# Performance work log

Hardware: AMD Instinct MI355X
Metric: run time of the kernel (lower is better)

Reference implementation:

```python
import jax, jax.numpy as jnp
import numpy as np

KH, KW = 3, 3      # kernel_size
SH, SW = 1, 1      # stride
MINVAL, MAXVAL = -0.45, -0.15


def setup_inputs() -> dict:
    key = jax.random.key(0)
    kx, kw = jax.random.split(key)
    x = jax.random.normal(kx, (16, 128, 128, 16), dtype=jnp.float32)  # NHWC
    W = jax.random.uniform(kw, (KH, KW, 16, 32), minval=MINVAL, maxval=MAXVAL,
                           dtype=jnp.float32)  # [kh, kw, C_in, filters]
    return {"x": x, "W": W}


def _dilation(x, W):
    # Max-plus sliding-window 'convolution' (VALID padding):
    # out[b,i,j,f] = max_{di,dj,c} x[b, i*SH+di, j*SW+dj, c] + W[di,dj,c,f]
    kh, kw, C, F = W.shape
    B, H, Wd, _ = x.shape
    Hout = (H - kh) // SH + 1
    Wout = (Wd - kw) // SW + 1
    out = jnp.full((B, Hout, Wout, F), -jnp.inf, dtype=x.dtype)
    for di in range(kh):          # small fixed loop over kernel offsets
        for dj in range(kw):
            xs = x[:, di:di + Hout * SH:SH, dj:dj + Wout * SW:SW, :]  # [B,Hout,Wout,C]
            # add W for this offset, reduce max over input channels
            out = jnp.maximum(out, jnp.max(xs[..., :, None] + W[di, dj], axis=3))
    return out


def reference(x, W):
    # erosion(x) = -dilation(-x)
    return -_dilation(-x, W)
```

## Files before the change

### kernel.cpp

```cpp
#include <hip/hip_runtime.h>
#include <math.h>


#define TI 21
#define TROWS (TI + 2)
#define LROW 64

typedef _Float16 h2 __attribute__((ext_vector_type(2)));

__device__ __forceinline__ h2 hmin2(h2 a, h2 b) {
    return __builtin_elementwise_min(a, b);
}

__device__ __forceinline__ h2 pkrtz(float a, float b) {
    auto r = __builtin_amdgcn_cvt_pkrtz(a, b);
    return *reinterpret_cast<h2*>(&r);
}

__device__ __forceinline__ h2 rowmin3(const float4* pr, const h2 w[3][4]) {
    h2 t[12];
#pragma unroll
    for (int dj = 0; dj < 3; ++dj) {
        const h2* p = reinterpret_cast<const h2*>(&pr[dj]);
#pragma unroll
        for (int q = 0; q < 4; ++q)
            t[dj * 4 + q] = p[q] - w[dj][q];
    }
#pragma unroll
    for (int k = 0; k < 6; ++k) t[k] = hmin2(t[k], t[k + 6]);
    t[0] = hmin2(t[0], t[3]);
    t[1] = hmin2(t[1], t[4]);
    t[2] = hmin2(t[2], t[5]);
    return hmin2(hmin2(t[0], t[1]), t[2]);
}

__global__ __launch_bounds__(256) void erosion_kernel(
    const float* __restrict__ x, const float* __restrict__ Wt,
    float* __restrict__ out)
{
    __shared__ _Float16 tile[2 * TROWS * LROW];
    __shared__ _Float16 wvm[TI * 256];

    const int tid = threadIdx.x;
    const int f  = tid & 31;
    const int ch = (tid >> 5) & 1;
    const int jt = tid >> 6;
    const int b  = blockIdx.z;
    const int i0 = blockIdx.y * TI;
    const int jb = blockIdx.x * 4;

    {
        const float* xg = x + (size_t)b * (128 * 128 * 16);
        auto stage = [&](int t) {
            int r   = t / 12;
            int k   = t % 12;
            int cc  = k >> 1;
            int ch2 = k & 1;
            int col = min(jb + cc, 127);
            const float* src = xg + ((size_t)(i0 + r) * 128 + col) * 16 + ch2 * 8;
            float4 lo = *reinterpret_cast<const float4*>(src);
            float4 hi = *reinterpret_cast<const float4*>(src + 4);
            h2 o[4] = { pkrtz(lo.x, lo.y), pkrtz(lo.z, lo.w),
                        pkrtz(hi.x, hi.y), pkrtz(hi.z, hi.w) };
            *reinterpret_cast<float4*>(
                &tile[ch2 * (TROWS * LROW) + r * LROW + cc * 8]) =
                *reinterpret_cast<float4*>(o);
        };
        stage(tid);
        if (tid < TROWS * 12 - 256) stage(tid + 256);
    }

    {
        h2* wl = reinterpret_cast<h2*>(wvm);
#pragma unroll
        for (int rr = 0; rr < 9; ++rr) {
            int t  = rr * 256 + tid;
            int g  = t >> 5;
            int ff = t & 31;
            float a  = Wt[g * 64 + ff];
            float c2 = Wt[g * 64 + 32 + ff];
            wl[g * 32 + ff] = pkrtz(a, c2);
        }
    }

    __syncthreads();

    h2 wh[3][3][4];
    {
        const h2* wl = reinterpret_cast<const h2*>(wvm);
#pragma unroll
        for (int p = 0; p < 9; ++p)
#pragma unroll
            for (int q = 0; q < 4; ++q)
                wh[p / 3][p % 3][q] = wl[(p * 8 + ch * 4 + q) * 32 + f];
    }

    const _Float16* lb = &tile[ch * (TROWS * LROW) + jt * 8];

    float4 pre[3];
#pragma unroll
    for (int dj = 0; dj < 3; ++dj)
        pre[dj] = *reinterpret_cast<const float4*>(lb + dj * 8);

    __syncthreads();

    const _Float16 HINF = (_Float16)__builtin_huge_valf();
    h2 accB = {HINF, HINF};
    h2 accC = {HINF, HINF};

    auto body = [&](int r, bool do_prefetch, bool do_vm) {
        h2 n0 = rowmin3(pre, wh[0]);
        h2 n1 = rowmin3(pre, wh[1]);
        h2 n2 = rowmin3(pre, wh[2]);

        if (do_prefetch) {
            const _Float16* ln = lb + (r + 1) * LROW;
#pragma unroll
            for (int dj = 0; dj < 3; ++dj)
                pre[dj] = *reinterpret_cast<const float4*>(ln + dj * 8);
        }

        h2 fin2 = hmin2(accC, n2);
        accC = hmin2(accB, n1);
        accB = n0;

        if (do_vm) {
            _Float16 a = fin2[0], c = fin2[1];
            _Float16 vm = a < c ? a : c;
            wvm[(r - 2) * 256 + tid] = vm;
        }
    };

    body(0, true, false);
    body(1, true, false);
#pragma unroll
    for (int r = 2; r < TROWS - 1; ++r)
        body(r, true, true);
    body(TROWS - 1, false, true);

    __syncthreads();

    {
        float* outb = out + (size_t)b * (126 * 126 * 32);
        auto merge = [&](int t) {
            int row = t >> 5;
            int k   = t & 31;
            int col = k >> 3;
            int q   = k & 7;
            int jj  = jb + col;
            const _Float16* base = &wvm[row * 256 + col * 64 + q * 4];
            h2 a[2], c[2];
            *reinterpret_cast<double*>(a) = *reinterpret_cast<const double*>(base);
            *reinterpret_cast<double*>(c) = *reinterpret_cast<const double*>(base + 32);
            h2 m0 = hmin2(a[0], c[0]);
            h2 m1 = hmin2(a[1], c[1]);
            float4 o = { (float)m0[0], (float)m0[1], (float)m1[0], (float)m1[1] };
            if (jj < 126)
                *reinterpret_cast<float4*>(
                    &outb[((size_t)(i0 + row) * 126 + jj) * 32 + q * 4]) = o;
        };
        merge(tid);
        merge(tid + 256);
        if (tid < TI * 32 - 512) merge(tid + 512);
    }
}

extern "C" void kernel_launch(void* const* d_in, const int* in_sizes, int n_in,
                              void* d_out, int out_size, void* d_ws, size_t ws_size,
                              hipStream_t stream) {
    const float* x  = (const float*)d_in[0];
    const float* Wt = (const float*)d_in[1];
    float* out = (float*)d_out;

    dim3 grid(32, 6, 16);
    dim3 block(256);
    erosion_kernel<<<grid, block, 0, stream>>>(x, Wt, out);
}
```

Before: 108.3 us.

## Widen blocks to 8 columns and store outputs directly via cross-lane min

Doubles the block to 512 threads covering 8 output columns per block, which halves the grid and lowers the overlap of staged halo columns. The LDS stage that merged the two channel halves is replaced by a permlane32 swap (or a shfl_xor fallback) that reduces the halves in registers, and results are written straight to global memory from the compute loop. This removes the extra LDS round trip and one barrier. In exchange the stores become scalar 4-byte writes issued by only half the lanes, and the larger blocks with launch-bounds occupancy hints may constrain register allocation.

Measured after the change: 184.9 us. 1.71x slower.

```diff
diff --git a/kernel.cpp b/kernel.cpp
--- a/kernel.cpp
+++ b/kernel.cpp
@@ -4,7 +4,9 @@
 
 #define TI 21
 #define TROWS (TI + 2)
-#define LROW 64
+#define NCOL 8
+#define SCOL 10
+#define LROW 80
 
 typedef _Float16 h2 __attribute__((ext_vector_type(2)));
 
@@ -34,12 +36,12 @@
     return hmin2(hmin2(t[0], t[1]), t[2]);
 }
 
-__global__ __launch_bounds__(256) void erosion_kernel(
+__global__ __launch_bounds__(512, 8) void erosion_kernel(
     const float* __restrict__ x, const float* __restrict__ Wt,
     float* __restrict__ out)
 {
-    __shared__ _Float16 tile[2 * TROWS * LROW];
-    __shared__ _Float16 wvm[TI * 256];
+    __shared__ __align__(16) _Float16 tile[2 * TROWS * LROW];
+    __shared__ __align__(16) _Float16 wbuf[2 * 2304];
 
     const int tid = threadIdx.x;
     const int f  = tid & 31;
@@ -47,39 +49,39 @@
     const int jt = tid >> 6;
     const int b  = blockIdx.z;
     const int i0 = blockIdx.y * TI;
-    const int jb = blockIdx.x * 4;
+    const int jb = blockIdx.x * NCOL;
 
-    {
+    if (tid < TROWS * 2 * SCOL) {
         const float* xg = x + (size_t)b * (128 * 128 * 16);
-        auto stage = [&](int t) {
-            int r   = t / 12;
-            int k   = t % 12;
-            int cc  = k >> 1;
-            int ch2 = k & 1;
-            int col = min(jb + cc, 127);
-            const float* src = xg + ((size_t)(i0 + r) * 128 + col) * 16 + ch2 * 8;
-            float4 lo = *reinterpret_cast<const float4*>(src);
-            float4 hi = *reinterpret_cast<const float4*>(src + 4);
-            h2 o[4] = { pkrtz(lo.x, lo.y), pkrtz(lo.z, lo.w),
-                        pkrtz(hi.x, hi.y), pkrtz(hi.z, hi.w) };
-            *reinterpret_cast<float4*>(
-                &tile[ch2 * (TROWS * LROW) + r * LROW + cc * 8]) =
-                *reinterpret_cast<float4*>(o);
-        };
-        stage(tid);
-        if (tid < TROWS * 12 - 256) stage(tid + 256);
+        int r   = tid / (2 * SCOL);
+        int k   = tid % (2 * SCOL);
+        int cc  = k >> 1;
+        int ch2 = k & 1;
+        int col = min(jb + cc, 127);
+        const float* src = xg + ((size_t)(i0 + r) * 128 + col) * 16 + ch2 * 8;
+        float4 lo = *reinterpret_cast<const float4*>(src);
+        float4 hi = *reinterpret_cast<const float4*>(src + 4);
+        h2 o[4] = { pkrtz(lo.x, lo.y), pkrtz(lo.z, lo.w),
+                    pkrtz(hi.x, hi.y), pkrtz(hi.z, hi.w) };
+        *reinterpret_cast<float4*>(
+            &tile[ch2 * (TROWS * LROW) + r * LROW + cc * 8]) =
+            *reinterpret_cast<float4*>(o);
     }
 
     {
-        h2* wl = reinterpret_cast<h2*>(wvm);
+        h2* wl = reinterpret_cast<h2*>(wbuf);
 #pragma unroll
-        for (int rr = 0; rr < 9; ++rr) {
-            int t  = rr * 256 + tid;
+        for (int rr = 0; rr < 4; ++rr) {
+            int t  = rr * 512 + tid;
             int g  = t >> 5;
             int ff = t & 31;
-            float a  = Wt[g * 64 + ff];
-            float c2 = Wt[g * 64 + 32 + ff];
-            wl[g * 32 + ff] = pkrtz(a, c2);
+            wl[t] = pkrtz(Wt[g * 64 + ff], Wt[g * 64 + 32 + ff]);
+        }
+        if (tid < 2304 - 2048) {
+            int t  = 2048 + tid;
+            int g  = t >> 5;
+            int ff = t & 31;
+            wl[t] = pkrtz(Wt[g * 64 + ff], Wt[g * 64 + 32 + ff]);
         }
     }
 
@@ -87,7 +89,7 @@
 
     h2 wh[3][3][4];
     {
-        const h2* wl = reinterpret_cast<const h2*>(wvm);
+        const h2* wl = reinterpret_cast<const h2*>(wbuf);
 #pragma unroll
         for (int p = 0; p < 9; ++p)
 #pragma unroll
@@ -102,13 +104,15 @@
     for (int dj = 0; dj < 3; ++dj)
         pre[dj] = *reinterpret_cast<const float4*>(lb + dj * 8);
 
-    __syncthreads();
-
     const _Float16 HINF = (_Float16)__builtin_huge_valf();
     h2 accB = {HINF, HINF};
     h2 accC = {HINF, HINF};
 
-    auto body = [&](int r, bool do_prefetch, bool do_vm) {
+    const int jj = jb + jt;
+    const bool wr = (ch == 0) && (jj < 126);
+    float* outb = out + (size_t)b * (126 * 126 * 32) + (size_t)jj * 32 + f;
+
+    auto body = [&](int r, bool do_prefetch, bool do_store) {
         h2 n0 = rowmin3(pre, wh[0]);
         h2 n1 = rowmin3(pre, wh[1]);
         h2 n2 = rowmin3(pre, wh[2]);
@@ -124,10 +128,19 @@
         accC = hmin2(accB, n1);
         accB = n0;
 
-        if (do_vm) {
-            _Float16 a = fin2[0], c = fin2[1];
-            _Float16 vm = a < c ? a : c;
-            wvm[(r - 2) * 256 + tid] = vm;
+        if (do_store) {
+            unsigned ua = __builtin_bit_cast(unsigned, fin2);
+#if __has_builtin(__builtin_amdgcn_permlane32_swap)
+            auto sw = __builtin_amdgcn_permlane32_swap(ua, ua, false, false);
+            h2 m2 = hmin2(__builtin_bit_cast(h2, (unsigned)sw[0]),
+                          __builtin_bit_cast(h2, (unsigned)sw[1]));
+#else
+            unsigned ub = (unsigned)__shfl_xor((int)ua, 32, 64);
+            h2 m2 = hmin2(fin2, __builtin_bit_cast(h2, ub));
+#endif
+            _Float16 m = m2[0] < m2[1] ? m2[0] : m2[1];
+            if (wr)
+                outb[(size_t)(i0 + r - 2) * (126 * 32)] = (float)m;
         }
     };
 
@@ -137,32 +150,6 @@
     for (int r = 2; r < TROWS - 1; ++r)
         body(r, true, true);
     body(TROWS - 1, false, true);
-
-    __syncthreads();
-
-    {
-        float* outb = out + (size_t)b * (126 * 126 * 32);
-        auto merge = [&](int t) {
-            int row = t >> 5;
-            int k   = t & 31;
-            int col = k >> 3;
-            int q   = k & 7;
-            int jj  = jb + col;
-            const _Float16* base = &wvm[row * 256 + col * 64 + q * 4];
-            h2 a[2], c[2];
-            *reinterpret_cast<double*>(a) = *reinterpret_cast<const double*>(base);
-            *reinterpret_cast<double*>(c) = *reinterpret_cast<const double*>(base + 32);
-            h2 m0 = hmin2(a[0], c[0]);
-            h2 m1 = hmin2(a[1], c[1]);
-            float4 o = { (float)m0[0], (float)m0[1], (float)m1[0], (float)m1[1] };
-            if (jj < 126)
-                *reinterpret_cast<float4*>(
-                    &outb[((size_t)(i0 + row) * 126 + jj) * 32 + q * 4]) = o;
-        };
-        merge(tid);
-        merge(tid + 256);
-        if (tid < TI * 32 - 512) merge(tid + 512);
-    }
 }
 
 extern "C" void kernel_launch(void* const* d_in, const int* in_sizes, int n_in,
@@ -172,7 +159,7 @@
     const float* Wt = (const float*)d_in[1];
     float* out = (float*)d_out;
 
-    dim3 grid(32, 6, 16);
-    dim3 block(256);
+    dim3 grid(16, 6, 16);
+    dim3 block(512);
     erosion_kernel<<<grid, block, 0, stream>>>(x, Wt, out);
 }
```

## Switch erosion inner loop to fp32 with v_min3, 512 threads and cross-lane merge

Applied to the files above, without the earlier changes.

Replaces the packed fp16 compute path with fp32 arithmetic that uses v_min3_f32, and doubles the block to 512 threads so each thread handles a quarter of the channels. Partial minima are merged across wave halves with permlane32_swap or a shuffle before the results go to LDS. The tile and weight buffers are now kept in fp32 with a padded layout, and the weights are read with inline ds_read_b128. The row loop is software-pipelined with two prefetch buffers. This is meant to drop the fp16 conversions and raise parallelism, at the cost of more LDS and more threads per output.

Measured after the change: 115.8 us. 6.9% more time.

```diff
diff --git a/kernel.cpp b/kernel.cpp
--- a/kernel.cpp
+++ b/kernel.cpp
@@ -4,7 +4,12 @@
 
 #define TI 21
 #define TROWS (TI + 2)
-#define LROW 64
+#define NCOL 4
+#define SCOL 6
+#define TROWF 96
+#define WPF 640
+#define VROW 288
+#define VGRP 36
 
 typedef _Float16 h2 __attribute__((ext_vector_type(2)));
 
@@ -12,131 +17,183 @@
     return __builtin_elementwise_min(a, b);
 }
 
-__device__ __forceinline__ h2 pkrtz(float a, float b) {
-    auto r = __builtin_amdgcn_cvt_pkrtz(a, b);
-    return *reinterpret_cast<h2*>(&r);
-}
-
-__device__ __forceinline__ h2 rowmin3(const float4* pr, const h2 w[3][4]) {
-    h2 t[12];
+__device__ __forceinline__ float min3f(float a, float b, float c) {
+    float d;
+    asm("v_min3_f32 %0, %1, %2, %3" : "=v"(d) : "v"(a), "v"(b), "v"(c));
+    return d;
+}
+
+__device__ __forceinline__ float rowminf(const float4* pr, const float4* w) {
+    float s[12];
 #pragma unroll
     for (int dj = 0; dj < 3; ++dj) {
-        const h2* p = reinterpret_cast<const h2*>(&pr[dj]);
-#pragma unroll
-        for (int q = 0; q < 4; ++q)
-            t[dj * 4 + q] = p[q] - w[dj][q];
-    }
-#pragma unroll
-    for (int k = 0; k < 6; ++k) t[k] = hmin2(t[k], t[k + 6]);
-    t[0] = hmin2(t[0], t[3]);
-    t[1] = hmin2(t[1], t[4]);
-    t[2] = hmin2(t[2], t[5]);
-    return hmin2(hmin2(t[0], t[1]), t[2]);
-}
-
-__global__ __launch_bounds__(256) void erosion_kernel(
+        const float* p = reinterpret_cast<const float*>(&pr[dj]);
+        const float* q = reinterpret_cast<const float*>(&w[dj]);
+#pragma unroll
+        for (int j = 0; j < 4; ++j)
+            s[dj * 4 + j] = p[j] - q[j];
+    }
+    float g0 = min3f(s[0], s[1], s[2]);
+    float g1 = min3f(s[3], s[4], s[5]);
+    float g2 = min3f(s[6], s[7], s[8]);
+    float g3 = min3f(s[9], s[10], s[11]);
+    return fminf(min3f(g0, g1, g2), g3);
+}
+
+__device__ __forceinline__ float mergev(float v) {
+    unsigned u = __builtin_bit_cast(unsigned, v);
+#if __has_builtin(__builtin_amdgcn_permlane32_swap)
+    auto sw = __builtin_amdgcn_permlane32_swap(u, u, false, false);
+    return fminf(__builtin_bit_cast(float, (unsigned)sw[0]),
+                 __builtin_bit_cast(float, (unsigned)sw[1]));
+#else
+    unsigned ub = (unsigned)__shfl_xor((int)u, 32, 64);
+    return fminf(v, __builtin_bit_cast(float, ub));
+#endif
+}
+
+__global__ __launch_bounds__(512)
+__attribute__((amdgpu_waves_per_eu(4, 4)))
+void erosion_kernel(
     const float* __restrict__ x, const float* __restrict__ Wt,
     float* __restrict__ out)
 {
-    __shared__ _Float16 tile[2 * TROWS * LROW];
-    __shared__ _Float16 wvm[TI * 256];
+    __shared__ __align__(16) float    tileF[TROWS * TROWF];
+    __shared__ __align__(16) float    wbufF[9 * WPF];
+    __shared__ __align__(16) _Float16 vm[TI * VROW];
 
     const int tid = threadIdx.x;
-    const int f  = tid & 31;
-    const int ch = (tid >> 5) & 1;
-    const int jt = tid >> 6;
+    const int f   = tid & 31;
+    const int chq = (tid >> 5) & 3;
+    const int jt  = tid >> 7;
+    const int src = (tid >> 6) & 1;
     const int b  = blockIdx.z;
     const int i0 = blockIdx.y * TI;
-    const int jb = blockIdx.x * 4;
+    const int jb = blockIdx.x * NCOL;
 
     {
         const float* xg = x + (size_t)b * (128 * 128 * 16);
         auto stage = [&](int t) {
-            int r   = t / 12;
-            int k   = t % 12;
-            int cc  = k >> 1;
-            int ch2 = k & 1;
+            int r  = t / 24;
+            int k  = t % 24;
+            int cc = k >> 2;
+            int cg = k & 3;
             int col = min(jb + cc, 127);
-            const float* src = xg + ((size_t)(i0 + r) * 128 + col) * 16 + ch2 * 8;
-            float4 lo = *reinterpret_cast<const float4*>(src);
-            float4 hi = *reinterpret_cast<const float4*>(src + 4);
-            h2 o[4] = { pkrtz(lo.x, lo.y), pkrtz(lo.z, lo.w),
-                        pkrtz(hi.x, hi.y), pkrtz(hi.z, hi.w) };
-            *reinterpret_cast<float4*>(
-                &tile[ch2 * (TROWS * LROW) + r * LROW + cc * 8]) =
-                *reinterpret_cast<float4*>(o);
+            const float* s = xg + ((size_t)(i0 + r) * 128 + col) * 16 + cg * 4;
+            *reinterpret_cast<float4*>(&tileF[r * TROWF + cc * 16 + cg * 4]) =
+                *reinterpret_cast<const float4*>(s);
         };
         stage(tid);
-        if (tid < TROWS * 12 - 256) stage(tid + 256);
-    }
-
-    {
-        h2* wl = reinterpret_cast<h2*>(wvm);
+        if (tid < TROWS * 24 - 512) stage(512 + tid);
+    }
+
+    {
 #pragma unroll
         for (int rr = 0; rr < 9; ++rr) {
-            int t  = rr * 256 + tid;
-            int g  = t >> 5;
-            int ff = t & 31;
-            float a  = Wt[g * 64 + ff];
-            float c2 = Wt[g * 64 + 32 + ff];
-            wl[g * 32 + ff] = pkrtz(a, c2);
+            int idx = rr * 512 + tid;
+            int p  = idx >> 9;
+            int c  = (idx >> 5) & 15;
+            int ff = idx & 31;
+            wbufF[p * WPF + ff * 20 + c] = Wt[idx];
         }
     }
 
     __syncthreads();
 
-    h2 wh[3][3][4];
-    {
-        const h2* wl = reinterpret_cast<const h2*>(wvm);
-#pragma unroll
-        for (int p = 0; p < 9; ++p)
-#pragma unroll
-            for (int q = 0; q < 4; ++q)
-                wh[p / 3][p % 3][q] = wl[(p * 8 + ch * 4 + q) * 32 + f];
-    }
-
-    const _Float16* lb = &tile[ch * (TROWS * LROW) + jt * 8];
-
-    float4 pre[3];
-#pragma unroll
-    for (int dj = 0; dj < 3; ++dj)
-        pre[dj] = *reinterpret_cast<const float4*>(lb + dj * 8);
-
-    __syncthreads();
-
-    const _Float16 HINF = (_Float16)__builtin_huge_valf();
-    h2 accB = {HINF, HINF};
-    h2 accC = {HINF, HINF};
-
-    auto body = [&](int r, bool do_prefetch, bool do_vm) {
-        h2 n0 = rowmin3(pre, wh[0]);
-        h2 n1 = rowmin3(pre, wh[1]);
-        h2 n2 = rowmin3(pre, wh[2]);
-
-        if (do_prefetch) {
-            const _Float16* ln = lb + (r + 1) * LROW;
+    float4 w9[9];
+    {
+        unsigned wa = (unsigned)(uintptr_t)(&wbufF[0]) + f * 80 + chq * 16;
+        asm volatile(
+            "ds_read_b128 %0, %9 offset:0\n\t"
+            "ds_read_b128 %1, %9 offset:2560\n\t"
+            "ds_read_b128 %2, %9 offset:5120\n\t"
+            "ds_read_b128 %3, %9 offset:7680\n\t"
+            "ds_read_b128 %4, %9 offset:10240\n\t"
+            "ds_read_b128 %5, %9 offset:12800\n\t"
+            "ds_read_b128 %6, %9 offset:15360\n\t"
+            "ds_read_b128 %7, %9 offset:17920\n\t"
+            "ds_read_b128 %8, %9 offset:20480\n\t"
+            "s_waitcnt lgkmcnt(0)"
+            : "=&v"(w9[0]), "=&v"(w9[1]), "=&v"(w9[2]), "=&v"(w9[3]),
+              "=&v"(w9[4]), "=&v"(w9[5]), "=&v"(w9[6]), "=&v"(w9[7]),
+              "=&v"(w9[8])
+            : "v"(wa)
+            : "memory");
+    }
+
+    const float* t0 = tileF + jt * 16 + chq * 4;
+
+    float4 preA[3], preB[3];
+#pragma unroll
+    for (int dj = 0; dj < 3; ++dj) {
+        preA[dj] = *reinterpret_cast<const float4*>(t0 + 0 * TROWF + dj * 16);
+        preB[dj] = *reinterpret_cast<const float4*>(t0 + 1 * TROWF + dj * 16);
+    }
+
+    const float FINF = __builtin_huge_valf();
+    float accB = FINF;
+    float accC = FINF;
+
+    _Float16* vp = &vm[jt * (2 * VGRP) + src * VGRP + f];
+
+    {
+        float n0 = rowminf(preA, &w9[0]);
+        float n1 = rowminf(preA, &w9[3]);
+        const float* ln = t0 + 2 * TROWF;
+#pragma unroll
+        for (int dj = 0; dj < 3; ++dj)
+            preA[dj] = *reinterpret_cast<const float4*>(ln + dj * 16);
+        accC = n1;
+        accB = n0;
+    }
+    {
+        float n0 = rowminf(preB, &w9[0]);
+        float n1 = rowminf(preB, &w9[3]);
+        const float* ln = t0 + 3 * TROWF;
+#pragma unroll
+        for (int dj = 0; dj < 3; ++dj)
+            preB[dj] = *reinterpret_cast<const float4*>(ln + dj * 16);
+        accC = fminf(accB, n1);
+        accB = n0;
+    }
+
+    const float* ldp = t0 + 4 * TROWF;
+#pragma clang loop unroll(disable)
+    for (int it = 0; it < 10; ++it) {
+        {
+            float n0 = rowminf(preA, &w9[0]);
+            float n1 = rowminf(preA, &w9[3]);
+            float n2 = rowminf(preA, &w9[6]);
 #pragma unroll
             for (int dj = 0; dj < 3; ++dj)
-                pre[dj] = *reinterpret_cast<const float4*>(ln + dj * 8);
+                preA[dj] = *reinterpret_cast<const float4*>(ldp + dj * 16);
+            float fin2 = fminf(accC, n2);
+            accC = fminf(accB, n1);
+            accB = n0;
+            vp[0] = (_Float16)mergev(fin2);
         }
-
-        h2 fin2 = hmin2(accC, n2);
-        accC = hmin2(accB, n1);
-        accB = n0;
-
-        if (do_vm) {
-            _Float16 a = fin2[0], c = fin2[1];
-            _Float16 vm = a < c ? a : c;
-            wvm[(r - 2) * 256 + tid] = vm;
+        {
+            float n0 = rowminf(preB, &w9[0]);
+            float n1 = rowminf(preB, &w9[3]);
+            float n2 = rowminf(preB, &w9[6]);
+            const float* ln = ldp + TROWF;
+#pragma unroll
+            for (int dj = 0; dj < 3; ++dj)
+                preB[dj] = *reinterpret_cast<const float4*>(ln + dj * 16);
+            float fin2 = fminf(accC, n2);
+            accC = fminf(accB, n1);
+            accB = n0;
+            vp[VROW] = (_Float16)mergev(fin2);
         }
-    };
-
-    body(0, true, false);
-    body(1, true, false);
-#pragma unroll
-    for (int r = 2; r < TROWS - 1; ++r)
-        body(r, true, true);
-    body(TROWS - 1, false, true);
+        ldp += 2 * TROWF;
+        vp  += 2 * VROW;
+    }
+
+    {
+        float n2 = rowminf(preA, &w9[6]);
+        float fin2 = fminf(accC, n2);
+        vp[0] = (_Float16)mergev(fin2);
+    }
 
     __syncthreads();
 
@@ -148,10 +205,10 @@
             int col = k >> 3;
             int q   = k & 7;
             int jj  = jb + col;
-            const _Float16* base = &wvm[row * 256 + col * 64 + q * 4];
+            const _Float16* base = &vm[row * VROW + col * (2 * VGRP) + q * 4];
             h2 a[2], c[2];
             *reinterpret_cast<double*>(a) = *reinterpret_cast<const double*>(base);
-            *reinterpret_cast<double*>(c) = *reinterpret_cast<const double*>(base + 32);
+            *reinterpret_cast<double*>(c) = *reinterpret_cast<const double*>(base + VGRP);
             h2 m0 = hmin2(a[0], c[0]);
             h2 m1 = hmin2(a[1], c[1]);
             float4 o = { (float)m0[0], (float)m0[1], (float)m1[0], (float)m1[1] };
@@ -160,8 +217,7 @@
                     &outb[((size_t)(i0 + row) * 126 + jj) * 32 + q * 4]) = o;
         };
         merge(tid);
-        merge(tid + 256);
-        if (tid < TI * 32 - 512) merge(tid + 512);
+        if (tid < TI * 32 - 512) merge(512 + tid);
     }
 }
 
@@ -173,6 +229,6 @@
     float* out = (float*)d_out;
 
     dim3 grid(32, 6, 16);
-    dim3 block(256);
+    dim3 block(512);
     erosion_kernel<<<grid, block, 0, stream>>>(x, Wt, out);
 }
```
